# Performance work log

Measured on AMD Instinct MI355X. Metric: run time of the kernel, lower is better.

## Reference

```python
import jax, jax.numpy as jnp
import numpy as np


def log_g(x):
    # Appendix B.3 of 'Were RNNs All We Needed?'
    return jnp.where(x >= 0, jnp.log(jax.nn.relu(x) + 0.5), -jax.nn.softplus(-x))


def parallel_scan_log(log_a, log_b):
    # h[0] = b[0]; h[i] = a[i]*h[i-1] + b[i], computed in log space along axis 1
    log_a_star = jnp.cumsum(log_a, axis=1)
    log_x0_plus_b_star = jax.lax.cumlogsumexp(log_b - log_a_star, axis=1)
    return jnp.exp(log_a_star + log_x0_plus_b_star)


def setup_inputs() -> dict:
    key = jax.random.key(0)
    B, T, D = 8, 4096, 1024
    k1, k2, k3, k4, k5 = jax.random.split(key, 5)
    scale = 1.0 / np.sqrt(D)
    return {
        "h_prev_layer": jax.random.normal(k1, (B, T, D), dtype=jnp.float32),
        "W_z": jax.random.uniform(k2, (D, D), jnp.float32, -scale, scale),
        "b_z": jax.random.uniform(k3, (D,), jnp.float32, -scale, scale),
        "W_h": jax.random.uniform(k4, (D, D), jnp.float32, -scale, scale),
        "b_h": jax.random.uniform(k5, (D,), jnp.float32, -scale, scale),
    }


def reference(h_prev_layer, W_z, b_z, W_h, b_h):
    k = jnp.einsum('btd,ed->bte', h_prev_layer, W_z) + b_z          # linear_z
    tilde_h = jnp.einsum('btd,ed->bte', h_prev_layer, W_h) + b_h    # linear_h
    log_z = -jax.nn.softplus(-k)
    log_one_minus_z = -jax.nn.softplus(k)
    log_tilde_h = log_g(tilde_h)
    return parallel_scan_log(log_one_minus_z, log_z + log_tilde_h)
```

## Files before the change

### kernel.cpp

```cpp
#include <hip/hip_runtime.h>
#include <hip/hip_fp16.h>

typedef float f32x4 __attribute__((ext_vector_type(4)));
typedef __bf16 bf16x8 __attribute__((ext_vector_type(8)));

#define BB_ 8
#define TT_ 4096
#define DD_ 1024
#define MM_ (BB_*TT_)
#define KK_ DD_

#define NCH 64
#define LCH (TT_/NCH)

static __device__ __forceinline__ unsigned short f2bf_rn(float f) {
  unsigned int u = __float_as_uint(f);
  u += 0x7FFFu + ((u >> 16) & 1u);
  return (unsigned short)(u >> 16);
}

__global__ void cvt_f32_bf16(const float4* __restrict__ src,
                             ushort4* __restrict__ dst, int n4) {
  int stride = gridDim.x * blockDim.x;
  for (int i = blockIdx.x * blockDim.x + threadIdx.x; i < n4; i += stride) {
    float4 v = src[i];
    ushort4 o;
    o.x = f2bf_rn(v.x); o.y = f2bf_rn(v.y);
    o.z = f2bf_rn(v.z); o.w = f2bf_rn(v.w);
    dst[i] = o;
  }
}

__global__ void cvt_w(const float4* __restrict__ Wz4,
                      const float4* __restrict__ Wh4,
                      ushort4* __restrict__ Wcat) {
  int flat = blockIdx.x * 256 + threadIdx.x;
  int mtx = flat >> 18;
  int j = flat & 262143;
  float4 v = (mtx ? Wh4 : Wz4)[j];
  int D = j >> 8;
  int kq = j & 255;
  int row = ((D >> 7) << 8) + (mtx << 7) + (D & 127);
  ushort4 o;
  o.x = f2bf_rn(v.x); o.y = f2bf_rn(v.y);
  o.z = f2bf_rn(v.z); o.w = f2bf_rn(v.w);
  Wcat[(size_t)row * 256 + kq] = o;
}

__device__ __forceinline__ void gload_lds16(const void* g, void* l) {
  __builtin_amdgcn_global_load_lds(
      (const __attribute__((address_space(1))) void*)g,
      (__attribute__((address_space(3))) void*)l, 16, 0, 0);
}

#define STA(q, nb_, kkh) gload_lds16(pXa + (q) * 65536 + (kkh), (nb_) + (q) * 8192 + wofs)
#define STB(q, nb_, kkh) gload_lds16(pWb + (q) * 65536 + (kkh), (nb_) + 32768 + (q) * 8192 + wofs)

#define PHASE(cb_, mh, kh, STAGEOPS, WAITOPS) do {                          \
    const char* Ab_ = (cb_);                                                \
    const char* Bb_ = (cb_) + 32768;                                        \
    const int sk_ = (kh) ? sk1 : sk0;                                       \
    bf16x8 af_[4];                                                          \
    _Pragma("unroll")                                                       \
    for (int ii = 0; ii < 4; ++ii)                                          \
      af_[ii] = *reinterpret_cast<const bf16x8*>(                           \
          Ab_ + rA7 + (mh) * 8192 + ii * 2048 + sk_);                       \
    if ((mh) == 0) {                                                        \
      _Pragma("unroll")                                                     \
      for (int j = 0; j < 4; ++j)                                           \
        bfv[j] = *reinterpret_cast<const bf16x8*>(                          \
            Bb_ + rB7 + j * 2048 + sk_);                                    \
    }                                                                       \
    STAGEOPS;                                                               \
    WAITOPS;                                                                \
    __builtin_amdgcn_s_barrier();                                           \
    asm volatile("s_waitcnt lgkmcnt(0)" ::: "memory");                      \
    __builtin_amdgcn_sched_barrier(0);                                      \
    __builtin_amdgcn_s_setprio(1);                                          \
    _Pragma("unroll")                                                       \
    for (int ii = 0; ii < 4; ++ii)                                          \
      _Pragma("unroll")                                                     \
      for (int j = 0; j < 4; ++j)                                           \
        acc[(mh) * 4 + ii][j] = __builtin_amdgcn_mfma_f32_16x16x32_bf16(    \
            af_[ii], bfv[j], acc[(mh) * 4 + ii][j], 0, 0, 0);               \
    __builtin_amdgcn_s_setprio(0);                                          \
    asm volatile("" ::: "memory");                                          \
    __builtin_amdgcn_s_barrier();                                           \
  } while (0)

__global__ __launch_bounds__(512, 2) void gemm_fused(
    const unsigned short* __restrict__ Xb,
    const unsigned short* __restrict__ Wb,
    const float* __restrict__ bz, const float* __restrict__ bh,
    __half* __restrict__ Zb, __half* __restrict__ Gb,
    float* __restrict__ Pp, float* __restrict__ Qq)
{
  extern __shared__ __align__(16) char smem[];
  const int tid  = threadIdx.x;
  const int wave = tid >> 6;
  const int lane = tid & 63;
  const int wm = wave >> 2, wn = wave & 3;
  const int fr = lane & 15, kg = lane >> 4;

  int swz = (blockIdx.x & 7) * 128 + (blockIdx.x >> 3);
  const int m0 = (swz >> 3) * 256;
  const int e0 = (swz & 7) * 256;
  const int dg = swz & 7;

  const int arow = tid >> 3;
  const int aslx = ((tid & 7) ^ (arow & 7)) * 8;
  const unsigned short* pXa = Xb + (size_t)(m0 + arow) * KK_ + aslx;
  const unsigned short* pWb = Wb + (size_t)(e0 + arow) * KK_ + aslx;
  const int wofs = wave * 1024;

  const int rA7 = (wm * 128 + fr) * 128;
  const int rB7 = (wn * 64 + fr) * 128;
  const int fx = fr & 7;
  const int sk0 = (kg ^ fx) * 16;
  const int sk1 = sk0 ^ 64;

  f32x4 acc[8][4];
  #pragma unroll
  for (int i = 0; i < 8; i++)
    #pragma unroll
    for (int j = 0; j < 4; j++)
      acc[i][j] = (f32x4){0.f, 0.f, 0.f, 0.f};
  bf16x8 bfv[4];

  STA(0, smem, 0); STA(2, smem, 0); STB(0, smem, 0);
  STB(1, smem, 0); STB(2, smem, 0); STB(3, smem, 0);
  STA(1, smem, 0); STA(3, smem, 0);
  asm volatile("s_waitcnt vmcnt(2)" ::: "memory");
  __builtin_amdgcn_s_barrier();

  #pragma unroll 1
  for (int t = 0; t < 15; ++t) {
    char* cb = smem + ((t & 1) << 16);
    char* nb = smem + (((t + 1) & 1) << 16);
    const int kn = (t + 1) * 64;
    PHASE(cb, 0, 0, {STA(0, nb, kn); STA(2, nb, kn); STB(0, nb, kn);},
          asm volatile("s_waitcnt vmcnt(3)" ::: "memory"));
    PHASE(cb, 1, 0, {STB(1, nb, kn); STB(2, nb, kn); STB(3, nb, kn);}, );
    PHASE(cb, 0, 1, {STA(1, nb, kn); STA(3, nb, kn);}, );
    PHASE(cb, 1, 1, {},
          asm volatile("s_waitcnt vmcnt(2)" ::: "memory"));
  }
  {
    char* cb = smem + 65536;
    PHASE(cb, 0, 0, {}, asm volatile("s_waitcnt vmcnt(0)" ::: "memory"));
    PHASE(cb, 1, 0, {}, );
    PHASE(cb, 0, 1, {}, );
    PHASE(cb, 1, 1, {}, );
  }

  __half* sc = (__half*)smem;
  const bool isZ = (wn < 2);
  const int dloc0 = (wn & 1) * 64;
  const int zg = isZ ? 0 : 1;
  const float* bias = isZ ? bz : bh;
  float bvv[4];
  #pragma unroll
  for (int j = 0; j < 4; ++j) bvv[j] = bias[dg * 128 + dloc0 + j * 16 + fr];

  #pragma unroll
  for (int a = 0; a < 8; ++a) {
    const int tl = wm * 128 + (a >> 2) * 64 + (a & 3) * 16 + kg * 4;
    #pragma unroll
    for (int j = 0; j < 4; ++j) {
      const int d = dloc0 + j * 16 + fr;
      #pragma unroll
      for (int r = 0; r < 4; ++r) {
        float val = acc[a][j][r] + bvv[j];
        float res;
        if (isZ) {
          res = 1.0f / (1.0f + __expf(-val));
        } else {
          res = (val >= 0.0f) ? (val + 0.5f)
                              : (1.0f / (1.0f + __expf(-val)));
        }
        const int t = tl + r;
        sc[t * 256 + ((d >> 2) ^ (t & 15)) * 8 + (d & 3) * 2 + zg] =
            __float2half(res);
      }
    }
  }
  __syncthreads();

  {
    const int dl = tid & 127, cgl = tid >> 7;
    const int dq = dl >> 2, dlo = (dl & 3) * 2;
    float pp = 1.f, qq = 0.f;
    #pragma unroll 4
    for (int i = 0; i < 64; ++i) {
      const int t = cgl * 64 + i;
      unsigned int zw = *reinterpret_cast<const unsigned int*>(
          &sc[t * 256 + ((dq ^ (t & 15)) * 8) + dlo]);
      float z = __half2float(__ushort_as_half((unsigned short)(zw & 0xffff)));
      float g = __half2float(__ushort_as_half((unsigned short)(zw >> 16)));
      float aa = 1.f - z;
      pp *= aa;
      qq = fmaf(aa, qq, z * g);
    }
    const int b = m0 >> 12;
    const int cg = ((m0 & 4095) >> 6) + cgl;
    size_t po = ((size_t)b * NCH + cg) * DD_ + dg * 128 + dl;
    Pp[po] = pp;
    Qq[po] = qq;
  }

  {
    const int row = tid >> 1, hd = tid & 1;
    const size_t rg = (size_t)m0 + row;
    __half* zdst = Zb + rg * DD_ + dg * 128 + hd * 64;
    __half* gdst = Gb + rg * DD_ + dg * 128 + hd * 64;
    const int t = row;
    #pragma unroll
    for (int k = 0; k < 8; ++k) {
      const int dq0 = hd * 16 + k * 2;
      uint4 i0 = *reinterpret_cast<const uint4*>(
          &sc[t * 256 + ((dq0 ^ (t & 15)) * 8)]);
      uint4 i1 = *reinterpret_cast<const uint4*>(
          &sc[t * 256 + (((dq0 + 1) ^ (t & 15)) * 8)]);
      uint4 zv, gv;
      zv.x = (i0.x & 0xffffu) | (i0.y << 16);
      zv.y = (i0.z & 0xffffu) | (i0.w << 16);
      zv.z = (i1.x & 0xffffu) | (i1.y << 16);
      zv.w = (i1.z & 0xffffu) | (i1.w << 16);
      gv.x = (i0.x >> 16) | (i0.y & 0xffff0000u);
      gv.y = (i0.z >> 16) | (i0.w & 0xffff0000u);
      gv.z = (i1.x >> 16) | (i1.y & 0xffff0000u);
      gv.w = (i1.z >> 16) | (i1.w & 0xffff0000u);
      *reinterpret_cast<uint4*>(zdst + k * 8) = zv;
      *reinterpret_cast<uint4*>(gdst + k * 8) = gv;
    }
  }
}

__global__ __launch_bounds__(256) void scan_combine(
    const float* __restrict__ P, const float* __restrict__ Q,
    float* __restrict__ H) {
  const int d = blockIdx.x * 256 + threadIdx.x;
  const int b = blockIdx.y;
  float h = 0.f;
  for (int c = 0; c < NCH; ++c) {
    size_t o = ((size_t)b * NCH + c) * DD_ + d;
    H[o] = h;
    h = fmaf(P[o], h, Q[o]);
  }
}

__global__ __launch_bounds__(256) void scan_apply(
    const ushort4* __restrict__ Z, const ushort4* __restrict__ G,
    const float4* __restrict__ H, float4* __restrict__ out) {
  const int d4 = threadIdx.x;
  const int c  = blockIdx.x;
  const int b  = blockIdx.y;
  float4 h = H[((size_t)b * NCH + c) * (DD_ / 4) + d4];
  size_t base = ((size_t)b * TT_ + (size_t)c * LCH) * (DD_ / 4) + d4;
  for (int t = 0; t < LCH; ++t) {
    ushort4 uz = Z[base + (size_t)t * (DD_ / 4)];
    ushort4 ug = G[base + (size_t)t * (DD_ / 4)];
    float z, g, a;
    z = __half2float(__ushort_as_half(uz.x)); g = __half2float(__ushort_as_half(ug.x));
    a = 1.f - z; h.x = fmaf(a, h.x, z * g);
    z = __half2float(__ushort_as_half(uz.y)); g = __half2float(__ushort_as_half(ug.y));
    a = 1.f - z; h.y = fmaf(a, h.y, z * g);
    z = __half2float(__ushort_as_half(uz.z)); g = __half2float(__ushort_as_half(ug.z));
    a = 1.f - z; h.z = fmaf(a, h.z, z * g);
    z = __half2float(__ushort_as_half(uz.w)); g = __half2float(__ushort_as_half(ug.w));
    a = 1.f - z; h.w = fmaf(a, h.w, z * g);
    out[base + (size_t)t * (DD_ / 4)] = h;
  }
}

extern "C" void kernel_launch(void* const* d_in, const int* in_sizes, int n_in,
                              void* d_out, int out_size, void* d_ws, size_t ws_size,
                              hipStream_t stream) {
  const float* X  = (const float*)d_in[0];
  const float* Wz = (const float*)d_in[1];
  const float* bz = (const float*)d_in[2];
  const float* Wh = (const float*)d_in[3];
  const float* bh = (const float*)d_in[4];
  float* out = (float*)d_out;

  const size_t szXb = (size_t)MM_ * DD_ * 2;
  const size_t szWb = (size_t)2 * DD_ * DD_ * 2;
  const size_t szZ  = (size_t)MM_ * DD_ * 2;
  const size_t szPQ = (size_t)BB_ * NCH * DD_ * 4;

  char* ws = (char*)d_ws;
  unsigned short *Xb, *Wb;
  __half *Zb, *Gb;
  const size_t needA = szXb + szWb + 2 * szZ + 3 * szPQ;
  if (ws_size >= needA) {
    Xb = (unsigned short*)ws;              ws += szXb;
    Wb = (unsigned short*)ws;              ws += szWb;
  } else {
    Xb = (unsigned short*)d_out;
    Wb = (unsigned short*)((char*)d_out + szXb);
  }
  Zb = (__half*)ws;  ws += szZ;
  Gb = (__half*)ws;  ws += szZ;
  float* P = (float*)ws;  ws += szPQ;
  float* Q = (float*)ws;  ws += szPQ;
  float* H = (float*)ws;

  cvt_f32_bf16<<<2048, 256, 0, stream>>>((const float4*)X, (ushort4*)Xb,
                                         (int)((size_t)MM_ * DD_ / 4));
  cvt_w<<<2048, 256, 0, stream>>>((const float4*)Wz, (const float4*)Wh,
                                  (ushort4*)Wb);
  gemm_fused<<<(MM_ / 256) * ((2 * DD_) / 256), 512, 131072, stream>>>(
      Xb, Wb, bz, bh, Zb, Gb, P, Q);

  scan_combine<<<dim3(4, BB_), 256, 0, stream>>>(P, Q, H);
  scan_apply<<<dim3(NCH, BB_), 256, 0, stream>>>((const ushort4*)Zb, (const ushort4*)Gb,
                                                 (const float4*)H, (float4*)out);
}
```

Baseline: 318.5 us.

## Interleave Z/H weights per wave and compute chunk scans in registers

```diff
diff --git a/kernel.cpp b/kernel.cpp
--- a/kernel.cpp
+++ b/kernel.cpp
@@ -40,11 +40,11 @@
   float4 v = (mtx ? Wh4 : Wz4)[j];
   int D = j >> 8;
   int kq = j & 255;
-  int row = ((D >> 7) << 8) + (mtx << 7) + (D & 127);
+  int e = ((D >> 5) << 6) + (mtx << 5) + (D & 31);
   ushort4 o;
   o.x = f2bf_rn(v.x); o.y = f2bf_rn(v.y);
   o.z = f2bf_rn(v.z); o.w = f2bf_rn(v.w);
-  Wcat[(size_t)row * 256 + kq] = o;
+  Wcat[(size_t)e * 256 + kq] = o;
 }
 
 __device__ __forceinline__ void gload_lds16(const void* g, void* l) {
@@ -92,7 +92,7 @@
     const unsigned short* __restrict__ Xb,
     const unsigned short* __restrict__ Wb,
     const float* __restrict__ bz, const float* __restrict__ bh,
-    __half* __restrict__ Zb, __half* __restrict__ Gb,
+    unsigned int* __restrict__ ZG,
     float* __restrict__ Pp, float* __restrict__ Qq)
 {
   extern __shared__ __align__(16) char smem[];
@@ -105,7 +105,6 @@
   int swz = (blockIdx.x & 7) * 128 + (blockIdx.x >> 3);
   const int m0 = (swz >> 3) * 256;
   const int e0 = (swz & 7) * 256;
-  const int dg = swz & 7;
 
   const int arow = tid >> 3;
   const int aslx = ((tid & 7) ^ (arow & 7)) * 8;
@@ -153,85 +152,66 @@
     PHASE(cb, 1, 1, {}, );
   }
 
-  __half* sc = (__half*)smem;
-  const bool isZ = (wn < 2);
-  const int dloc0 = (wn & 1) * 64;
-  const int zg = isZ ? 0 : 1;
-  const float* bias = isZ ? bz : bh;
-  float bvv[4];
+  const int dw0 = (swz & 7) * 128 + wn * 32;
+  const int t0 = m0 & 4095;
+  const int bidx = m0 >> 12;
+
+  float bzv[2], bhv[2];
   #pragma unroll
-  for (int j = 0; j < 4; ++j) bvv[j] = bias[dg * 128 + dloc0 + j * 16 + fr];
+  for (int j = 0; j < 2; ++j) {
+    bzv[j] = bz[dw0 + j * 16 + fr];
+    bhv[j] = bh[dw0 + j * 16 + fr];
+  }
+
+  unsigned int* ew = (unsigned int*)(smem + wave * 9216);
+  const int sub = lane & 7, rowr = lane >> 3;
 
   #pragma unroll
-  for (int a = 0; a < 8; ++a) {
-    const int tl = wm * 128 + (a >> 2) * 64 + (a & 3) * 16 + kg * 4;
+  for (int p = 0; p < 2; ++p) {
+    float PP[2] = {1.f, 1.f}, QQ[2] = {0.f, 0.f};
     #pragma unroll
-    for (int j = 0; j < 4; ++j) {
-      const int d = dloc0 + j * 16 + fr;
+    for (int ii = 0; ii < 4; ++ii) {
       #pragma unroll
-      for (int r = 0; r < 4; ++r) {
-        float val = acc[a][j][r] + bvv[j];
-        float res;
-        if (isZ) {
-          res = 1.0f / (1.0f + __expf(-val));
-        } else {
-          res = (val >= 0.0f) ? (val + 0.5f)
-                              : (1.0f / (1.0f + __expf(-val)));
+      for (int j = 0; j < 2; ++j) {
+        float segP = 1.f, segQ = 0.f;
+        #pragma unroll
+        for (int r = 0; r < 4; ++r) {
+          float kz = acc[p * 4 + ii][j][r] + bzv[j];
+          float th = acc[p * 4 + ii][j + 2][r] + bhv[j];
+          float z = 1.0f / (1.0f + __expf(-kz));
+          float g = (th >= 0.0f) ? (th + 0.5f)
+                                 : (1.0f / (1.0f + __expf(-th)));
+          unsigned int pk =
+              (unsigned int)__half_as_ushort(__float2half(z)) |
+              ((unsigned int)__half_as_ushort(__float2half(g)) << 16);
+          ew[(ii * 16 + kg * 4 + r) * 36 + j * 16 + fr] = pk;
+          float aa = 1.f - z;
+          segP *= aa;
+          segQ = fmaf(aa, segQ, z * g);
         }
-        const int t = tl + r;
-        sc[t * 256 + ((d >> 2) ^ (t & 15)) * 8 + (d & 3) * 2 + zg] =
-            __float2half(res);
+        float p1 = __shfl_down(segP, 16), q1 = __shfl_down(segQ, 16);
+        segQ = fmaf(p1, segQ, q1); segP *= p1;
+        float p2 = __shfl_down(segP, 32), q2 = __shfl_down(segQ, 32);
+        segQ = fmaf(p2, segQ, q2); segP *= p2;
+        QQ[j] = fmaf(segP, QQ[j], segQ);
+        PP[j] *= segP;
       }
     }
-  }
-  __syncthreads();
-
-  {
-    const int dl = tid & 127, cgl = tid >> 7;
-    const int dq = dl >> 2, dlo = (dl & 3) * 2;
-    float pp = 1.f, qq = 0.f;
-    #pragma unroll 4
-    for (int i = 0; i < 64; ++i) {
-      const int t = cgl * 64 + i;
-      unsigned int zw = *reinterpret_cast<const unsigned int*>(
-          &sc[t * 256 + ((dq ^ (t & 15)) * 8) + dlo]);
-      float z = __half2float(__ushort_as_half((unsigned short)(zw & 0xffff)));
-      float g = __half2float(__ushort_as_half((unsigned short)(zw >> 16)));
-      float aa = 1.f - z;
-      pp *= aa;
-      qq = fmaf(aa, qq, z * g);
+    if (kg == 0) {
+      const int cg = (t0 >> 6) + wm * 2 + p;
+      #pragma unroll
+      for (int j = 0; j < 2; ++j) {
+        size_t po = ((size_t)bidx * NCH + cg) * DD_ + dw0 + j * 16 + fr;
+        Pp[po] = PP[j];
+        Qq[po] = QQ[j];
+      }
     }
-    const int b = m0 >> 12;
-    const int cg = ((m0 & 4095) >> 6) + cgl;
-    size_t po = ((size_t)b * NCH + cg) * DD_ + dg * 128 + dl;
-    Pp[po] = pp;
-    Qq[po] = qq;
-  }
-
-  {
-    const int row = tid >> 1, hd = tid & 1;
-    const size_t rg = (size_t)m0 + row;
-    __half* zdst = Zb + rg * DD_ + dg * 128 + hd * 64;
-    __half* gdst = Gb + rg * DD_ + dg * 128 + hd * 64;
-    const int t = row;
     #pragma unroll
-    for (int k = 0; k < 8; ++k) {
-      const int dq0 = hd * 16 + k * 2;
-      uint4 i0 = *reinterpret_cast<const uint4*>(
-          &sc[t * 256 + ((dq0 ^ (t & 15)) * 8)]);
-      uint4 i1 = *reinterpret_cast<const uint4*>(
-          &sc[t * 256 + (((dq0 + 1) ^ (t & 15)) * 8)]);
-      uint4 zv, gv;
-      zv.x = (i0.x & 0xffffu) | (i0.y << 16);
-      zv.y = (i0.z & 0xffffu) | (i0.w << 16);
-      zv.z = (i1.x & 0xffffu) | (i1.y << 16);
-      zv.w = (i1.z & 0xffffu) | (i1.w << 16);
-      gv.x = (i0.x >> 16) | (i0.y & 0xffff0000u);
-      gv.y = (i0.z >> 16) | (i0.w & 0xffff0000u);
-      gv.z = (i1.x >> 16) | (i1.y & 0xffff0000u);
-      gv.w = (i1.z >> 16) | (i1.w & 0xffff0000u);
-      *reinterpret_cast<uint4*>(zdst + k * 8) = zv;
-      *reinterpret_cast<uint4*>(gdst + k * 8) = gv;
+    for (int q = 0; q < 8; ++q) {
+      int rl = q * 8 + rowr;
+      uint4 v = *reinterpret_cast<const uint4*>(&ew[rl * 36 + sub * 4]);
+      size_t rg = (size_t)(m0 + wm * 128 + p * 64 + rl);
+      *reinterpret_cast<uint4*>(&ZG[rg * DD_ + dw0 + sub * 4]) = v;
     }
   }
 }
@@ -250,24 +230,27 @@
 }
 
 __global__ __launch_bounds__(256) void scan_apply(
-    const ushort4* __restrict__ Z, const ushort4* __restrict__ G,
-    const float4* __restrict__ H, float4* __restrict__ out) {
+    const uint4* __restrict__ ZG, const float4* __restrict__ H,
+    float4* __restrict__ out) {
   const int d4 = threadIdx.x;
   const int c  = blockIdx.x;
   const int b  = blockIdx.y;
   float4 h = H[((size_t)b * NCH + c) * (DD_ / 4) + d4];
   size_t base = ((size_t)b * TT_ + (size_t)c * LCH) * (DD_ / 4) + d4;
   for (int t = 0; t < LCH; ++t) {
-    ushort4 uz = Z[base + (size_t)t * (DD_ / 4)];
-    ushort4 ug = G[base + (size_t)t * (DD_ / 4)];
+    uint4 w = ZG[base + (size_t)t * (DD_ / 4)];
     float z, g, a;
-    z = __half2float(__ushort_as_half(uz.x)); g = __half2float(__ushort_as_half(ug.x));
+    z = __half2float(__ushort_as_half((unsigned short)(w.x & 0xffff)));
+    g = __half2float(__ushort_as_half((unsigned short)(w.x >> 16)));
     a = 1.f - z; h.x = fmaf(a, h.x, z * g);
-    z = __half2float(__ushort_as_half(uz.y)); g = __half2float(__ushort_as_half(ug.y));
+    z = __half2float(__ushort_as_half((unsigned short)(w.y & 0xffff)));
+    g = __half2float(__ushort_as_half((unsigned short)(w.y >> 16)));
     a = 1.f - z; h.y = fmaf(a, h.y, z * g);
-    z = __half2float(__ushort_as_half(uz.z)); g = __half2float(__ushort_as_half(ug.z));
+    z = __half2float(__ushort_as_half((unsigned short)(w.z & 0xffff)));
+    g = __half2float(__ushort_as_half((unsigned short)(w.z >> 16)));
     a = 1.f - z; h.z = fmaf(a, h.z, z * g);
-    z = __half2float(__ushort_as_half(uz.w)); g = __half2float(__ushort_as_half(ug.w));
+    z = __half2float(__ushort_as_half((unsigned short)(w.w & 0xffff)));
+    g = __half2float(__ushort_as_half((unsigned short)(w.w >> 16)));
     a = 1.f - z; h.w = fmaf(a, h.w, z * g);
     out[base + (size_t)t * (DD_ / 4)] = h;
   }
@@ -285,13 +268,12 @@
 
   const size_t szXb = (size_t)MM_ * DD_ * 2;
   const size_t szWb = (size_t)2 * DD_ * DD_ * 2;
-  const size_t szZ  = (size_t)MM_ * DD_ * 2;
+  const size_t szZG = (size_t)MM_ * DD_ * 4;
   const size_t szPQ = (size_t)BB_ * NCH * DD_ * 4;
 
   char* ws = (char*)d_ws;
   unsigned short *Xb, *Wb;
-  __half *Zb, *Gb;
-  const size_t needA = szXb + szWb + 2 * szZ + 3 * szPQ;
+  const size_t needA = szXb + szWb + szZG + 3 * szPQ;
   if (ws_size >= needA) {
     Xb = (unsigned short*)ws;              ws += szXb;
     Wb = (unsigned short*)ws;              ws += szWb;
@@ -299,8 +281,7 @@
     Xb = (unsigned short*)d_out;
     Wb = (unsigned short*)((char*)d_out + szXb);
   }
-  Zb = (__half*)ws;  ws += szZ;
-  Gb = (__half*)ws;  ws += szZ;
+  unsigned int* ZG = (unsigned int*)ws;  ws += szZG;
   float* P = (float*)ws;  ws += szPQ;
   float* Q = (float*)ws;  ws += szPQ;
   float* H = (float*)ws;
@@ -310,9 +291,9 @@
   cvt_w<<<2048, 256, 0, stream>>>((const float4*)Wz, (const float4*)Wh,
                                   (ushort4*)Wb);
   gemm_fused<<<(MM_ / 256) * ((2 * DD_) / 256), 512, 131072, stream>>>(
-      Xb, Wb, bz, bh, Zb, Gb, P, Q);
+      Xb, Wb, bz, bh, ZG, P, Q);
 
   scan_combine<<<dim3(4, BB_), 256, 0, stream>>>(P, Q, H);
-  scan_apply<<<dim3(NCH, BB_), 256, 0, stream>>>((const ushort4*)Zb, (const ushort4*)Gb,
+  scan_apply<<<dim3(NCH, BB_), 256, 0, stream>>>((const uint4*)ZG,
                                                  (const float4*)H, (float4*)out);
 }
```

Result: faster. 264.1 us (-17.1%).
